# Performance work log

Hardware: AMD Instinct MI355X
Metric: run time of the kernel (lower is better)

Reference implementation:

```python
import jax, jax.numpy as jnp
import numpy as np

K_MASK = -2.3819763e+38
NUM_HEADS = 16
NUM_KV_HEADS = 8
HEAD_DIM = 128
FEATURES = 2048
QUERY_SCALE = 0.08838834764831845  # head_dim ** -0.5
ROPE_BASE = 10000
SOFT_CAP = 50.0
WINDOW = 1024


def apply_rope(inputs, positions, base_frequency=ROPE_BASE):
    # inputs: [B, L, N, H], positions: [B, L]
    head_dim = inputs.shape[-1]
    fraction = 2.0 * jnp.arange(0, head_dim // 2, dtype=jnp.float32) / head_dim
    timescale = jnp.asarray(base_frequency, jnp.float32) ** fraction
    sinusoid = positions[..., None].astype(jnp.float32) / timescale[None, None, :]
    sinusoid = sinusoid[..., None, :]  # [B, L, 1, H/2]
    sin, cos = jnp.sin(sinusoid), jnp.cos(sinusoid)
    first, second = jnp.split(inputs, 2, axis=-1)
    out = jnp.concatenate([first * cos - second * sin,
                           second * cos + first * sin], axis=-1)
    return out.astype(inputs.dtype)


def setup_inputs() -> dict:
    key = jax.random.key(0)
    ks = jax.random.split(key, 4)
    B, T, D = 2, 2048, FEATURES
    x = jax.random.normal(ks[0], (B, T, D), dtype=jnp.float32)
    segment_pos = jnp.broadcast_to(jnp.arange(T, dtype=jnp.int32)[None, :], (B, T))
    # causal prefill mask [B, T, S] with S == T
    attn_mask = jnp.broadcast_to(
        jnp.tril(jnp.ones((T, T), dtype=bool))[None], (B, T, T))
    wq = jax.random.normal(ks[1], (NUM_HEADS, D, HEAD_DIM), dtype=jnp.float32) * 0.02
    wkv = jax.random.normal(ks[2], (2, NUM_KV_HEADS, D, HEAD_DIM), dtype=jnp.float32) * 0.02
    wo = jax.random.normal(ks[3], (NUM_HEADS, HEAD_DIM, D), dtype=jnp.float32) * 0.02
    return {"x": x, "segment_pos": segment_pos, "attn_mask": attn_mask,
            "wq": wq, "wkv": wkv, "wo": wo}


def reference(x, segment_pos, attn_mask, wq, wkv, wo):
    # Projections
    q = jnp.einsum('BTD,NDH->BTNH', x, wq)              # [B,T,N,H]
    kv = jnp.einsum('BSD,CKDH->CBSKH', x, wkv)          # [2,B,S,K,H]
    k, v = kv[0], kv[1]

    # RoPE + query scaling
    q = apply_rope(q, segment_pos) * QUERY_SCALE
    k = apply_rope(k, segment_pos)

    # GQA: fold query heads into (K groups, G heads per group)
    B, T, N, H = q.shape
    K, G = NUM_KV_HEADS, N // NUM_KV_HEADS
    qg = q.reshape(B, T, K, G, H)
    logits = jnp.einsum('BTKGH,BSKH->BTKGS', qg, k).reshape(B, T, N, -1)

    # Logit soft-capping
    logits = jnp.tanh(logits / SOFT_CAP) * SOFT_CAP

    # Sliding-window mask (prefill: end_index=0, cache_len = S)
    S = attn_mask.shape[-1]
    cache_positions = jnp.arange(S)[None, None, :]       # [1,1,S]
    sp = segment_pos[:, :, None]                         # [B,T,1]
    sliding = (cache_positions > sp - WINDOW) & (cache_positions < sp + WINDOW)
    mask = jnp.logical_and(attn_mask, sliding)

    padded = jnp.where(mask[:, :, None, :], logits, K_MASK)
    probs = jax.nn.softmax(padded, axis=-1).astype(k.dtype)

    pg = probs.reshape(B, T, K, G, S)
    encoded = jnp.einsum('BTKGS,BSKH->BTKGH', pg, v).reshape(B, T, N, H)
    return jnp.einsum('BTNH,NHD->BTD', encoded, wo)
```

## Files before the change

kernel.cpp:

```cpp
#include <hip/hip_runtime.h>

typedef __attribute__((ext_vector_type(8))) short short8;
typedef __attribute__((ext_vector_type(4))) float f32x4;
typedef __attribute__((ext_vector_type(4))) float f4;
typedef __attribute__((ext_vector_type(4))) unsigned short u16x4;

__device__ __forceinline__ unsigned short f2bf(float f) {
    union { float f; unsigned int u; } v; v.f = f;
    unsigned int r = v.u + 0x7fffu + ((v.u >> 16) & 1u);
    return (unsigned short)(r >> 16);
}
__device__ __forceinline__ float bf2f(unsigned short h) {
    union { unsigned int u; float f; } v; v.u = ((unsigned int)h) << 16;
    return v.f;
}
__device__ __forceinline__ void gload_lds16(const void* g, void* l) {
    __builtin_amdgcn_global_load_lds(
        (const __attribute__((address_space(1))) unsigned int*)g,
        (__attribute__((address_space(3))) unsigned int*)l, 16, 0, 0);
}


__global__ void conv_x(const float* __restrict__ x, unsigned short* __restrict__ xb) {
    int i = blockIdx.x * 256 + threadIdx.x;
    f4 v = ((const f4*)x)[i];
    u16x4 o;
    o[0] = f2bf(v[0]); o[1] = f2bf(v[1]); o[2] = f2bf(v[2]); o[3] = f2bf(v[3]);
    ((u16x4*)xb)[i] = o;
}

__global__ void conv_wqkvt(const float* __restrict__ wq, const float* __restrict__ wkv,
                           unsigned short* __restrict__ wt) {
    __shared__ float tile[64 * 65];
    const int d0 = blockIdx.x * 64, f0 = blockIdx.y * 64;
    const int head = f0 >> 7;
    const int h0 = f0 & 127;
    const float* src;
    float scl;
    if (head < 16) { src = wq + (size_t)head * 2048 * 128; scl = 0.08838834764831845f; }
    else           { src = wkv + (size_t)(head - 16) * 2048 * 128; scl = 1.f; }
    {
        int hh = threadIdx.x & 63, dq = threadIdx.x >> 6;
        #pragma unroll
        for (int r = 0; r < 16; ++r) {
            int dd = r * 4 + dq;
            tile[dd * 65 + hh] = src[(size_t)(d0 + dd) * 128 + h0 + hh] * scl;
        }
    }
    __syncthreads();
    {
        int dd = threadIdx.x & 63, fq = threadIdx.x >> 6;
        #pragma unroll
        for (int r = 0; r < 16; ++r) {
            int fl = r * 4 + fq;
            wt[(size_t)(f0 + fl) * 2048 + d0 + dd] = f2bf(tile[dd * 65 + fl]);
        }
    }
}

__global__ void conv_wot(const float* __restrict__ wo, unsigned short* __restrict__ wt) {
    __shared__ float tile[64 * 65];
    const int d0 = blockIdx.x * 64, r0 = blockIdx.y * 64;
    int cc = threadIdx.x & 63, rq = threadIdx.x >> 6;
    #pragma unroll
    for (int r = 0; r < 16; ++r) {
        int rr = r * 4 + rq;
        tile[rr * 65 + cc] = wo[(size_t)(r0 + rr) * 2048 + d0 + cc];
    }
    __syncthreads();
    #pragma unroll
    for (int r = 0; r < 16; ++r) {
        int rr = r * 4 + rq;
        wt[(size_t)(d0 + rr) * 2048 + r0 + cc] = f2bf(tile[cc * 65 + rr]);
    }
}


__global__ __launch_bounds__(512, 2)
void gemm8p(const unsigned short* __restrict__ A,
            const unsigned short* __restrict__ Bt,
            unsigned short* __restrict__ C,
            int ldk, int ldc, int nt, int ksplit, size_t cstride) {
    __shared__ __align__(16) unsigned short LDS[65536];
    const int tid = threadIdx.x, lane = tid & 63, w = tid >> 6;
    const int wr = w >> 2, wc = w & 3;
    const int l15 = lane & 15, l4 = lane >> 4;
    int nwg = gridDim.x * gridDim.y;
    int wg = blockIdx.y * gridDim.x + blockIdx.x;
    int swz = (wg & 7) * (nwg >> 3) + (wg >> 3);
    int bx = swz % gridDim.x, by = swz / gridDim.x;
    int slice = 0;
    if (ksplit) { slice = by & 1; by >>= 1; }
    unsigned short* Cs = C + (size_t)slice * cstride;
    const int brow = by * 256, bcol = bx * 256;
    const size_t koff = (size_t)slice * nt * 64;
    const int wg_a = w & 3;
    const int wg_b = wr;
    const int rA = wg_a * 8 + (lane >> 3);
    const int rB = wg_b * 8 + (lane >> 3);
    const int cgS = ((lane & 7) ^ (lane >> 3)) * 8;
    const unsigned short* aP = A + (size_t)(brow + wr * 128 + rA) * ldk + koff + cgS;
    const unsigned short* bP = Bt + (size_t)(bcol + wc * 64 + rB) * ldk + koff + cgS;
    const int ldsA0 = wr * 8192 + (wg_a * 64 + lane) * 8;
    const int ldsB0 = wc * 4096 + (wg_b * 64 + lane) * 8;
    const int aRd = (wr * 128 + l15) * 64;
    const int bRd = (wc * 64 + l15) * 64;
    const int c0 = ((0 + l4) ^ (l15 & 7)) * 8;
    const int c1 = ((4 + l4) ^ (l15 & 7)) * 8;
    f32x4 acc[8][4] = {};
    gload_lds16(aP,                    &LDS[ldsA0]);
    gload_lds16(bP,                    &LDS[16384 + ldsB0]);
    gload_lds16(aP + (size_t)32 * ldk, &LDS[ldsA0 + 2048]);
    gload_lds16(bP + (size_t)16 * ldk, &LDS[16384 + ldsB0 + 1024]);
    gload_lds16(bP + (size_t)32 * ldk, &LDS[16384 + ldsB0 + 2048]);
    gload_lds16(bP + (size_t)48 * ldk, &LDS[16384 + ldsB0 + 3072]);
    gload_lds16(aP + (size_t)64 * ldk, &LDS[ldsA0 + 4096]);
    gload_lds16(aP + (size_t)96 * ldk, &LDS[ldsA0 + 6144]);
    asm volatile("s_waitcnt vmcnt(4)" ::: "memory");
    __builtin_amdgcn_s_barrier();
    __builtin_amdgcn_sched_barrier(0);

    short8 af[4][2], bl[2][2], bh[2][2];
    for (int t = 0; t < nt; ++t) {
        const int bufA = (t & 1) << 15, bufB = bufA + 16384;
        const bool pf = (t + 1) < nt;
        const int sA = ((t + 1) & 1) << 15, sB = sA + 16384;
        const unsigned short* ap = aP + (t + 1) * 64;
        const unsigned short* bp = bP + (t + 1) * 64;
        #pragma unroll
        for (int m = 0; m < 4; ++m) {
            af[m][0] = *(const short8*)&LDS[bufA + aRd + m * 1024 + c0];
            af[m][1] = *(const short8*)&LDS[bufA + aRd + m * 1024 + c1];
        }
        #pragma unroll
        for (int n = 0; n < 2; ++n) {
            bl[n][0] = *(const short8*)&LDS[bufB + bRd + n * 1024 + c0];
            bl[n][1] = *(const short8*)&LDS[bufB + bRd + n * 1024 + c1];
        }
        if (pf) { gload_lds16(ap, &LDS[sA + ldsA0]);
                  gload_lds16(bp, &LDS[sB + ldsB0]); }
        __builtin_amdgcn_s_barrier();
        __builtin_amdgcn_sched_barrier(0);
        __builtin_amdgcn_s_setprio(1);
        #pragma unroll
        for (int kk = 0; kk < 2; ++kk)
            #pragma unroll
            for (int m = 0; m < 4; ++m)
                #pragma unroll
                for (int n = 0; n < 2; ++n)
                    acc[m][n] = __builtin_amdgcn_mfma_f32_16x16x32_bf16(af[m][kk], bl[n][kk], acc[m][n], 0, 0, 0);
        __builtin_amdgcn_s_setprio(0);
        asm volatile("s_waitcnt vmcnt(4)" ::: "memory");
        __builtin_amdgcn_s_barrier();
        __builtin_amdgcn_sched_barrier(0);
        #pragma unroll
        for (int n = 0; n < 2; ++n) {
            bh[n][0] = *(const short8*)&LDS[bufB + bRd + (n + 2) * 1024 + c0];
            bh[n][1] = *(const short8*)&LDS[bufB + bRd + (n + 2) * 1024 + c1];
        }
        if (pf) { gload_lds16(ap + (size_t)32 * ldk, &LDS[sA + ldsA0 + 2048]);
                  gload_lds16(bp + (size_t)16 * ldk, &LDS[sB + ldsB0 + 1024]); }
        __builtin_amdgcn_s_barrier();
        __builtin_amdgcn_sched_barrier(0);
        __builtin_amdgcn_s_setprio(1);
        #pragma unroll
        for (int kk = 0; kk < 2; ++kk)
            #pragma unroll
            for (int m = 0; m < 4; ++m)
                #pragma unroll
                for (int n = 0; n < 2; ++n)
                    acc[m][n + 2] = __builtin_amdgcn_mfma_f32_16x16x32_bf16(af[m][kk], bh[n][kk], acc[m][n + 2], 0, 0, 0);
        __builtin_amdgcn_s_setprio(0);
        asm volatile("s_waitcnt vmcnt(4)" ::: "memory");
        __builtin_amdgcn_s_barrier();
        __builtin_amdgcn_sched_barrier(0);
        #pragma unroll
        for (int m = 0; m < 4; ++m) {
            af[m][0] = *(const short8*)&LDS[bufA + aRd + (m + 4) * 1024 + c0];
            af[m][1] = *(const short8*)&LDS[bufA + aRd + (m + 4) * 1024 + c1];
        }
        if (pf) { gload_lds16(bp + (size_t)32 * ldk, &LDS[sB + ldsB0 + 2048]);
                  gload_lds16(bp + (size_t)48 * ldk, &LDS[sB + ldsB0 + 3072]); }
        __builtin_amdgcn_s_barrier();
        __builtin_amdgcn_sched_barrier(0);
        __builtin_amdgcn_s_setprio(1);
        #pragma unroll
        for (int kk = 0; kk < 2; ++kk)
            #pragma unroll
            for (int m = 0; m < 4; ++m)
                #pragma unroll
                for (int n = 0; n < 2; ++n)
                    acc[m + 4][n] = __builtin_amdgcn_mfma_f32_16x16x32_bf16(af[m][kk], bl[n][kk], acc[m + 4][n], 0, 0, 0);
        __builtin_amdgcn_s_setprio(0);
        __builtin_amdgcn_s_barrier();
        __builtin_amdgcn_sched_barrier(0);
        if (pf) { gload_lds16(ap + (size_t)64 * ldk, &LDS[sA + ldsA0 + 4096]);
                  gload_lds16(ap + (size_t)96 * ldk, &LDS[sA + ldsA0 + 6144]); }
        __builtin_amdgcn_s_barrier();
        __builtin_amdgcn_sched_barrier(0);
        __builtin_amdgcn_s_setprio(1);
        #pragma unroll
        for (int kk = 0; kk < 2; ++kk)
            #pragma unroll
            for (int m = 0; m < 4; ++m)
                #pragma unroll
                for (int n = 0; n < 2; ++n)
                    acc[m + 4][n + 2] = __builtin_amdgcn_mfma_f32_16x16x32_bf16(af[m][kk], bh[n][kk], acc[m + 4][n + 2], 0, 0, 0);
        __builtin_amdgcn_s_setprio(0);
        asm volatile("s_waitcnt vmcnt(4)" ::: "memory");
        __builtin_amdgcn_s_barrier();
        __builtin_amdgcn_sched_barrier(0);
    }
    #pragma unroll
    for (int m = 0; m < 8; ++m)
        #pragma unroll
        for (int n = 0; n < 4; ++n)
            #pragma unroll
            for (int j = 0; j < 4; ++j) {
                int row = brow + wr * 128 + m * 16 + l4 * 4 + j;
                int col = bcol + wc * 64 + n * 16 + l15;
                Cs[(size_t)row * ldc + col] = f2bf(acc[m][n][j]);
            }
}

__global__ void addparts(const unsigned short* __restrict__ p0,
                         const unsigned short* __restrict__ p1,
                         float* __restrict__ out) {
    int i = blockIdx.x * 256 + threadIdx.x;
    short8 a = ((const short8*)p0)[i];
    short8 b = ((const short8*)p1)[i];
    f4 lo, hi;
    #pragma unroll
    for (int j = 0; j < 4; ++j)
        lo[j] = bf2f((unsigned short)a[j]) + bf2f((unsigned short)b[j]);
    #pragma unroll
    for (int j = 0; j < 4; ++j)
        hi[j] = bf2f((unsigned short)a[j + 4]) + bf2f((unsigned short)b[j + 4]);
    ((f4*)out)[2 * i] = lo;
    ((f4*)out)[2 * i + 1] = hi;
}

__global__ void rope_reshape(const unsigned short* __restrict__ qkv,
                             const int* __restrict__ segpos,
                             unsigned short* __restrict__ q_r,
                             unsigned short* __restrict__ k_r) {
    const int bt = blockIdx.x;
    const int hd = blockIdx.y * 2 + (threadIdx.x >> 7);
    const int b = bt >> 11, t = bt & 2047;
    const int h = threadIdx.x & 127;
    const unsigned short* in = (hd < 16)
        ? qkv + (size_t)bt * 4096 + hd * 128
        : qkv + (size_t)bt * 4096 + 2048 + (hd - 16) * 128;
    int pos = segpos[bt];
    int i = h & 63;
    float inv_ts = __expf((float)i * (-9.210340371976184f / 64.f));
    float ang = (float)pos * inv_ts;
    float s = __sinf(ang), c = __cosf(ang);
    float x1 = bf2f(in[i]);
    float x2 = bf2f(in[i + 64]);
    float o = (h < 64) ? (x1 * c - x2 * s) : (x2 * c + x1 * s);
    if (hd < 16) {
        q_r[((size_t)((b * 16 + hd) * 2048 + t)) * 128 + h] = f2bf(o);
    } else {
        int kh = hd - 16;
        k_r[((size_t)((b * 8 + kh) * 2048 + t)) * 128 + h] = f2bf(o);
    }
}

__global__ void v_transpose(const unsigned short* __restrict__ qkv,
                            unsigned short* __restrict__ v_t) {
    __shared__ unsigned short tile[64][72];
    const int tt0 = blockIdx.x * 64;
    const int kh = blockIdx.y >> 1, hb = (blockIdx.y & 1) * 64;
    const int b = blockIdx.z;
    int c = threadIdx.x & 63, rq = threadIdx.x >> 6;
    #pragma unroll
    for (int r = 0; r < 16; ++r) {
        int tt = r * 4 + rq;
        tile[tt][c] = qkv[(size_t)(b * 2048 + tt0 + tt) * 4096 + 3072 + kh * 128 + hb + c];
    }
    __syncthreads();
    #pragma unroll
    for (int r = 0; r < 16; ++r) {
        int hr = r * 4 + rq;
        v_t[((size_t)(b * 8 + kh) * 128 + hb + hr) * 2048 + tt0 + c] = tile[c][hr];
    }
}


__device__ __forceinline__ void stage_kv(const unsigned short* kbase, const unsigned short* vbase,
                                         unsigned short* Ksb, unsigned short* Vtb,
                                         int st, int tid) {
    #pragma unroll
    for (int r = 0; r < 2; ++r) {
        int e = (r * 512 + tid) * 8;
        int krow = e >> 7, kcol = e & 127;
        gload_lds16(kbase + (size_t)(st * 64 + krow) * 128 + (kcol ^ ((krow & 7) << 3)), Ksb + e);
        int vrow = e >> 6, vcol = e & 63;
        gload_lds16(vbase + (size_t)vrow * 2048 + st * 64 + (vcol ^ ((vrow & 7) << 3)), Vtb + e);
    }
}

__global__ __launch_bounds__(512, 4)
void attn_kernel(const unsigned short* __restrict__ q_r,
                 const unsigned short* __restrict__ k_r,
                 const unsigned short* __restrict__ v_t,
                 unsigned short* __restrict__ enc) {
    __shared__ __align__(16) unsigned short Ks[2][64 * 128];
    __shared__ __align__(16) unsigned short Vt[2][128 * 64];
    __shared__ __align__(16) unsigned short Pl[8][16 * 64];
    const int tid = threadIdx.x, lane = tid & 63, wave = tid >> 6;
    const int l15 = lane & 15, l4 = lane >> 4;
    const int flat = blockIdx.x;
    const int xcd = flat & 7, g = flat >> 3;
    const int pair = xcd * 2 + (g >> 5);
    const int qb = 31 - (g & 31);
    const int kh = pair >> 1, b = pair & 1;
    const int n = kh * 2 + (wave >> 2);
    const int wq = wave & 3;
    short8 qf[4];
    {
        const unsigned short* qp =
            q_r + ((size_t)((b * 16 + n) * 2048 + qb * 64 + wq * 16 + l15)) * 128 + l4 * 8;
        #pragma unroll
        for (int kk = 0; kk < 4; ++kk) qf[kk] = *(const short8*)(qp + kk * 32);
    }
    f32x4 Of[8] = {};
    float lrow[4] = {};
    int t_lo = qb * 64 - 1023; if (t_lo < 0) t_lo = 0;
    const int st0 = t_lo >> 6;
    const unsigned short* kbase = k_r + (size_t)(b * 8 + kh) * 2048 * 128;
    const unsigned short* vbase = v_t + (size_t)(b * 8 + kh) * 128 * 2048;

    stage_kv(kbase, vbase, Ks[0], Vt[0], st0, tid);
    __syncthreads();
    int cur = 0;
    for (int st = st0; st <= qb; ++st) {
        if (st < qb)
            stage_kv(kbase, vbase, Ks[cur ^ 1], Vt[cur ^ 1], st + 1, tid);
        f32x4 sf[4] = {};
        #pragma unroll
        for (int nc = 0; nc < 4; ++nc) {
            int row = nc * 16 + l15;
            int sw = (l15 & 7) << 3;
            #pragma unroll
            for (int kk = 0; kk < 4; ++kk) {
                short8 bfr = *(const short8*)&Ks[cur][row * 128 + ((kk * 32 + l4 * 8) ^ sw)];
                sf[nc] = __builtin_amdgcn_mfma_f32_16x16x32_bf16(qf[kk], bfr, sf[nc], 0, 0, 0);
            }
        }
        const int mode = (st == qb) ? 1 : ((qb >= 16 && st == st0) ? 2 : 0);
        #pragma unroll
        for (int j = 0; j < 4; ++j) {
            int trow = qb * 64 + wq * 16 + l4 * 4 + j;
            int prow = l4 * 4 + j;
            int psw = (prow & 7) << 3;
            #pragma unroll
            for (int nc = 0; nc < 4; ++nc) {
                float ex = __expf(sf[nc][j] * 0.04f);
                float p = __expf(-100.f * __builtin_amdgcn_rcpf(ex + 1.f));
                if (mode) {
                    int s = st * 64 + nc * 16 + l15;
                    bool ok = (mode == 1) ? (s <= trow) : (s >= trow - 1023);
                    p = ok ? p : 0.f;
                }
                lrow[j] += p;
                Pl[wave][prow * 64 + ((nc * 16 + l15) ^ psw)] = f2bf(p);
            }
        }
        {
            int asw = (l15 & 7) << 3;
            #pragma unroll
            for (int ks = 0; ks < 2; ++ks) {
                short8 af = *(const short8*)&Pl[wave][l15 * 64 + ((ks * 32 + l4 * 8) ^ asw)];
                #pragma unroll
                for (int hc = 0; hc < 8; ++hc) {
                    int vrow = hc * 16 + l15;
                    short8 bfr = *(const short8*)&Vt[cur][vrow * 64 + ((ks * 32 + l4 * 8) ^ asw)];
                    Of[hc] = __builtin_amdgcn_mfma_f32_16x16x32_bf16(af, bfr, Of[hc], 0, 0, 0);
                }
            }
        }
        __syncthreads();
        cur ^= 1;
    }
    float inv[4];
    #pragma unroll
    for (int j = 0; j < 4; ++j) {
        float l = lrow[j];
        l += __shfl_xor(l, 1); l += __shfl_xor(l, 2);
        l += __shfl_xor(l, 4); l += __shfl_xor(l, 8);
        inv[j] = 1.f / l;
    }
    #pragma unroll
    for (int hc = 0; hc < 8; ++hc)
        #pragma unroll
        for (int j = 0; j < 4; ++j) {
            size_t row = (size_t)(b * 2048 + qb * 64 + wq * 16 + l4 * 4 + j);
            enc[row * 2048 + n * 128 + hc * 16 + l15] = f2bf(Of[hc][j] * inv[j]);
        }
}


extern "C" void kernel_launch(void* const* d_in, const int* in_sizes, int n_in,
                              void* d_out, int out_size, void* d_ws, size_t ws_size,
                              hipStream_t stream) {
    const float* x   = (const float*)d_in[0];
    const int* segp  = (const int*)d_in[1];
    const float* wq  = (const float*)d_in[3];
    const float* wkv = (const float*)d_in[4];
    const float* wo  = (const float*)d_in[5];
    float* out = (float*)d_out;
    char* ws = (char*)d_ws;
    if (ws_size < ((size_t)96 << 20)) return;

    unsigned short* xb    = (unsigned short*)(ws);
    unsigned short* wqkvt = (unsigned short*)(ws + ((size_t)16 << 20));
    unsigned short* qkv   = (unsigned short*)(ws + ((size_t)32 << 20));
    unsigned short* q_r   = (unsigned short*)(ws + ((size_t)64 << 20));
    unsigned short* k_r   = (unsigned short*)(ws + ((size_t)80 << 20));
    unsigned short* v_t   = (unsigned short*)(ws + ((size_t)88 << 20));
    unsigned short* wo_t  = (unsigned short*)(ws + ((size_t)16 << 20));
    unsigned short* enc   = (unsigned short*)(ws + ((size_t)32 << 20));
    unsigned short* part  = (unsigned short*)(ws + ((size_t)64 << 20));

    conv_x<<<8192, 256, 0, stream>>>(x, xb);
    conv_wqkvt<<<dim3(32, 64), 256, 0, stream>>>(wq, wkv, wqkvt);
    gemm8p<<<dim3(16, 16), 512, 0, stream>>>(xb, wqkvt, qkv, 2048, 4096, 32, 0, 0);
    rope_reshape<<<dim3(4096, 12), 256, 0, stream>>>(qkv, segp, q_r, k_r);
    v_transpose<<<dim3(32, 16, 2), 256, 0, stream>>>(qkv, v_t);
    conv_wot<<<dim3(32, 32), 256, 0, stream>>>(wo, wo_t);
    attn_kernel<<<512, 512, 0, stream>>>(q_r, k_r, v_t, enc);
    gemm8p<<<dim3(8, 32), 512, 0, stream>>>(enc, wo_t, part, 2048, 2048, 16, 1, (size_t)4096 * 2048);
    addparts<<<4096, 256, 0, stream>>>(part, part + (size_t)4096 * 2048, out);
}
```

Before: 216.2 us.

## Deepen GEMM prefetch to two tiles ahead and streamline attention exp

```diff
diff --git a/kernel.cpp b/kernel.cpp
--- a/kernel.cpp
+++ b/kernel.cpp
@@ -13,6 +13,9 @@
 __device__ __forceinline__ float bf2f(unsigned short h) {
     union { unsigned int u; float f; } v; v.u = ((unsigned int)h) << 16;
     return v.f;
+}
+__device__ __forceinline__ float fexp2(float x) {
+    float r; asm("v_exp_f32 %0, %1" : "=v"(r) : "v"(x)); return r;
 }
 __device__ __forceinline__ void gload_lds16(const void* g, void* l) {
     __builtin_amdgcn_global_load_lds(
@@ -116,17 +119,28 @@
     gload_lds16(bP + (size_t)48 * ldk, &LDS[16384 + ldsB0 + 3072]);
     gload_lds16(aP + (size_t)64 * ldk, &LDS[ldsA0 + 4096]);
     gload_lds16(aP + (size_t)96 * ldk, &LDS[ldsA0 + 6144]);
-    asm volatile("s_waitcnt vmcnt(4)" ::: "memory");
+    {
+        const unsigned short* a1 = aP + 64;
+        const unsigned short* b1 = bP + 64;
+        gload_lds16(a1,                    &LDS[32768 + ldsA0]);
+        gload_lds16(b1,                    &LDS[49152 + ldsB0]);
+        gload_lds16(a1 + (size_t)32 * ldk, &LDS[32768 + ldsA0 + 2048]);
+        gload_lds16(b1 + (size_t)16 * ldk, &LDS[49152 + ldsB0 + 1024]);
+        gload_lds16(b1 + (size_t)32 * ldk, &LDS[49152 + ldsB0 + 2048]);
+        gload_lds16(b1 + (size_t)48 * ldk, &LDS[49152 + ldsB0 + 3072]);
+    }
+    asm volatile("s_waitcnt vmcnt(6)" ::: "memory");
     __builtin_amdgcn_s_barrier();
     __builtin_amdgcn_sched_barrier(0);
 
     short8 af[4][2], bl[2][2], bh[2][2];
-    for (int t = 0; t < nt; ++t) {
+    for (int t = 0; t < nt - 1; ++t) {
         const int bufA = (t & 1) << 15, bufB = bufA + 16384;
-        const bool pf = (t + 1) < nt;
-        const int sA = ((t + 1) & 1) << 15, sB = sA + 16384;
-        const unsigned short* ap = aP + (t + 1) * 64;
-        const unsigned short* bp = bP + (t + 1) * 64;
+        const int sA = ((t + 1) & 1) << 15;
+        const bool pf2 = (t + 2) < nt;
+        const unsigned short* ap1 = aP + (size_t)(t + 1) * 64;
+        const unsigned short* ap2 = aP + (size_t)(t + 2) * 64;
+        const unsigned short* bp2 = bP + (size_t)(t + 2) * 64;
         #pragma unroll
         for (int m = 0; m < 4; ++m) {
             af[m][0] = *(const short8*)&LDS[bufA + aRd + m * 1024 + c0];
@@ -137,8 +151,8 @@
             bl[n][0] = *(const short8*)&LDS[bufB + bRd + n * 1024 + c0];
             bl[n][1] = *(const short8*)&LDS[bufB + bRd + n * 1024 + c1];
         }
-        if (pf) { gload_lds16(ap, &LDS[sA + ldsA0]);
-                  gload_lds16(bp, &LDS[sB + ldsB0]); }
+        gload_lds16(ap1 + (size_t)64 * ldk, &LDS[sA + ldsA0 + 4096]);
+        gload_lds16(ap1 + (size_t)96 * ldk, &LDS[sA + ldsA0 + 6144]);
         __builtin_amdgcn_s_barrier();
         __builtin_amdgcn_sched_barrier(0);
         __builtin_amdgcn_s_setprio(1);
@@ -150,7 +164,7 @@
                 for (int n = 0; n < 2; ++n)
                     acc[m][n] = __builtin_amdgcn_mfma_f32_16x16x32_bf16(af[m][kk], bl[n][kk], acc[m][n], 0, 0, 0);
         __builtin_amdgcn_s_setprio(0);
-        asm volatile("s_waitcnt vmcnt(4)" ::: "memory");
+        asm volatile("s_waitcnt vmcnt(6)" ::: "memory");
         __builtin_amdgcn_s_barrier();
         __builtin_amdgcn_sched_barrier(0);
         #pragma unroll
@@ -158,8 +172,8 @@
             bh[n][0] = *(const short8*)&LDS[bufB + bRd + (n + 2) * 1024 + c0];
             bh[n][1] = *(const short8*)&LDS[bufB + bRd + (n + 2) * 1024 + c1];
         }
-        if (pf) { gload_lds16(ap + (size_t)32 * ldk, &LDS[sA + ldsA0 + 2048]);
-                  gload_lds16(bp + (size_t)16 * ldk, &LDS[sB + ldsB0 + 1024]); }
+        if (pf2) { gload_lds16(ap2, &LDS[bufA + ldsA0]);
+                   gload_lds16(bp2, &LDS[bufB + ldsB0]); }
         __builtin_amdgcn_s_barrier();
         __builtin_amdgcn_sched_barrier(0);
         __builtin_amdgcn_s_setprio(1);
@@ -171,7 +185,7 @@
                 for (int n = 0; n < 2; ++n)
                     acc[m][n + 2] = __builtin_amdgcn_mfma_f32_16x16x32_bf16(af[m][kk], bh[n][kk], acc[m][n + 2], 0, 0, 0);
         __builtin_amdgcn_s_setprio(0);
-        asm volatile("s_waitcnt vmcnt(4)" ::: "memory");
+        asm volatile("s_waitcnt vmcnt(6)" ::: "memory");
         __builtin_amdgcn_s_barrier();
         __builtin_amdgcn_sched_barrier(0);
         #pragma unroll
@@ -179,8 +193,8 @@
             af[m][0] = *(const short8*)&LDS[bufA + aRd + (m + 4) * 1024 + c0];
             af[m][1] = *(const short8*)&LDS[bufA + aRd + (m + 4) * 1024 + c1];
         }
-        if (pf) { gload_lds16(bp + (size_t)32 * ldk, &LDS[sB + ldsB0 + 2048]);
-                  gload_lds16(bp + (size_t)48 * ldk, &LDS[sB + ldsB0 + 3072]); }
+        if (pf2) { gload_lds16(ap2 + (size_t)32 * ldk, &LDS[bufA + ldsA0 + 2048]);
+                   gload_lds16(bp2 + (size_t)16 * ldk, &LDS[bufB + ldsB0 + 1024]); }
         __builtin_amdgcn_s_barrier();
         __builtin_amdgcn_sched_barrier(0);
         __builtin_amdgcn_s_setprio(1);
@@ -192,10 +206,11 @@
                 for (int n = 0; n < 2; ++n)
                     acc[m + 4][n] = __builtin_amdgcn_mfma_f32_16x16x32_bf16(af[m][kk], bl[n][kk], acc[m + 4][n], 0, 0, 0);
         __builtin_amdgcn_s_setprio(0);
-        __builtin_amdgcn_s_barrier();
-        __builtin_amdgcn_sched_barrier(0);
-        if (pf) { gload_lds16(ap + (size_t)64 * ldk, &LDS[sA + ldsA0 + 4096]);
-                  gload_lds16(ap + (size_t)96 * ldk, &LDS[sA + ldsA0 + 6144]); }
+        asm volatile("s_waitcnt vmcnt(6)" ::: "memory");
+        __builtin_amdgcn_s_barrier();
+        __builtin_amdgcn_sched_barrier(0);
+        if (pf2) { gload_lds16(bp2 + (size_t)32 * ldk, &LDS[bufB + ldsB0 + 2048]);
+                   gload_lds16(bp2 + (size_t)48 * ldk, &LDS[bufB + ldsB0 + 3072]); }
         __builtin_amdgcn_s_barrier();
         __builtin_amdgcn_sched_barrier(0);
         __builtin_amdgcn_s_setprio(1);
@@ -207,9 +222,49 @@
                 for (int n = 0; n < 2; ++n)
                     acc[m + 4][n + 2] = __builtin_amdgcn_mfma_f32_16x16x32_bf16(af[m][kk], bh[n][kk], acc[m + 4][n + 2], 0, 0, 0);
         __builtin_amdgcn_s_setprio(0);
-        asm volatile("s_waitcnt vmcnt(4)" ::: "memory");
-        __builtin_amdgcn_s_barrier();
-        __builtin_amdgcn_sched_barrier(0);
+        asm volatile("s_waitcnt vmcnt(6)" ::: "memory");
+        __builtin_amdgcn_s_barrier();
+        __builtin_amdgcn_sched_barrier(0);
+    }
+    asm volatile("s_waitcnt vmcnt(0)" ::: "memory");
+    __builtin_amdgcn_s_barrier();
+    {
+        const int bufA = ((nt - 1) & 1) << 15, bufB = bufA + 16384;
+        #pragma unroll
+        for (int m = 0; m < 4; ++m) {
+            af[m][0] = *(const short8*)&LDS[bufA + aRd + m * 1024 + c0];
+            af[m][1] = *(const short8*)&LDS[bufA + aRd + m * 1024 + c1];
+        }
+        #pragma unroll
+        for (int n = 0; n < 2; ++n) {
+            bl[n][0] = *(const short8*)&LDS[bufB + bRd + n * 1024 + c0];
+            bl[n][1] = *(const short8*)&LDS[bufB + bRd + n * 1024 + c1];
+            bh[n][0] = *(const short8*)&LDS[bufB + bRd + (n + 2) * 1024 + c0];
+            bh[n][1] = *(const short8*)&LDS[bufB + bRd + (n + 2) * 1024 + c1];
+        }
+        #pragma unroll
+        for (int kk = 0; kk < 2; ++kk)
+            #pragma unroll
+            for (int m = 0; m < 4; ++m)
+                #pragma unroll
+                for (int n = 0; n < 2; ++n) {
+                    acc[m][n]     = __builtin_amdgcn_mfma_f32_16x16x32_bf16(af[m][kk], bl[n][kk], acc[m][n], 0, 0, 0);
+                    acc[m][n + 2] = __builtin_amdgcn_mfma_f32_16x16x32_bf16(af[m][kk], bh[n][kk], acc[m][n + 2], 0, 0, 0);
+                }
+        #pragma unroll
+        for (int m = 0; m < 4; ++m) {
+            af[m][0] = *(const short8*)&LDS[bufA + aRd + (m + 4) * 1024 + c0];
+            af[m][1] = *(const short8*)&LDS[bufA + aRd + (m + 4) * 1024 + c1];
+        }
+        #pragma unroll
+        for (int kk = 0; kk < 2; ++kk)
+            #pragma unroll
+            for (int m = 0; m < 4; ++m)
+                #pragma unroll
+                for (int n = 0; n < 2; ++n) {
+                    acc[m + 4][n]     = __builtin_amdgcn_mfma_f32_16x16x32_bf16(af[m][kk], bl[n][kk], acc[m + 4][n], 0, 0, 0);
+                    acc[m + 4][n + 2] = __builtin_amdgcn_mfma_f32_16x16x32_bf16(af[m][kk], bh[n][kk], acc[m + 4][n + 2], 0, 0, 0);
+                }
     }
     #pragma unroll
     for (int m = 0; m < 8; ++m)
@@ -339,6 +394,7 @@
         if (st < qb)
             stage_kv(kbase, vbase, Ks[cur ^ 1], Vt[cur ^ 1], st + 1, tid);
         f32x4 sf[4] = {};
+        __builtin_amdgcn_s_setprio(1);
         #pragma unroll
         for (int nc = 0; nc < 4; ++nc) {
             int row = nc * 16 + l15;
@@ -349,6 +405,7 @@
                 sf[nc] = __builtin_amdgcn_mfma_f32_16x16x32_bf16(qf[kk], bfr, sf[nc], 0, 0, 0);
             }
         }
+        __builtin_amdgcn_s_setprio(0);
         const int mode = (st == qb) ? 1 : ((qb >= 16 && st == st0) ? 2 : 0);
         #pragma unroll
         for (int j = 0; j < 4; ++j) {
@@ -357,8 +414,8 @@
             int psw = (prow & 7) << 3;
             #pragma unroll
             for (int nc = 0; nc < 4; ++nc) {
-                float ex = __expf(sf[nc][j] * 0.04f);
-                float p = __expf(-100.f * __builtin_amdgcn_rcpf(ex + 1.f));
+                float ex = fexp2(sf[nc][j] * 0.057707801635558534f);
+                float p = fexp2(-144.26950408889634f * __builtin_amdgcn_rcpf(ex + 1.f));
                 if (mode) {
                     int s = st * 64 + nc * 16 + l15;
                     bool ok = (mode == 1) ? (s <= trow) : (s >= trow - 1023);
@@ -370,6 +427,7 @@
         }
         {
             int asw = (l15 & 7) << 3;
+            __builtin_amdgcn_s_setprio(1);
             #pragma unroll
             for (int ks = 0; ks < 2; ++ks) {
                 short8 af = *(const short8*)&Pl[wave][l15 * 64 + ((ks * 32 + l4 * 8) ^ asw)];
@@ -380,6 +438,7 @@
                     Of[hc] = __builtin_amdgcn_mfma_f32_16x16x32_bf16(af, bfr, Of[hc], 0, 0, 0);
                 }
             }
+            __builtin_amdgcn_s_setprio(0);
         }
         __syncthreads();
         cur ^= 1;
```

Result: no change. 215.1 us (-0.5%).
